# Performance work log

Measured on AMD Instinct MI355X. Metric: run time of the kernel, lower is better.

Reference implementation:

```python
import jax, jax.numpy as jnp
import numpy as np

INF = jnp.float32(1e9)


def _nearest_zero_dist_axis0(is_zero):
    """1D distance (in index units) to the nearest True along axis 0.

    is_zero: bool array [L, ...]. Returns float32 [L, ...].
    """
    d0 = jnp.where(is_zero, jnp.float32(0.0), INF)

    def step(c, d):
        c = jnp.minimum(c + 1.0, d)
        return c, c

    init = jnp.full(d0.shape[1:], INF, dtype=jnp.float32)
    _, fwd = jax.lax.scan(step, init, d0)
    _, bwd = jax.lax.scan(step, init, d0[::-1])
    return jnp.minimum(fwd, bwd[::-1])


def _minplus_parabola_axis0(g2):
    """Exact squared-EDT lower envelope along axis 0.

    g2: float32 [L, ...] of squared distances. Returns
    out[i, ...] = min_k ( (i-k)^2 + g2[k, ...] ).
    Brute-force min-plus, scanned over output index to bound memory.
    """
    L = g2.shape[0]
    k = jnp.arange(L, dtype=jnp.float32)

    def step(_, i):
        # (i - k)^2 broadcast against all source positions k
        par = (i - k) ** 2  # [L]
        par = par.reshape((L,) + (1,) * (g2.ndim - 1))
        return None, jnp.min(par + g2, axis=0)  # [...]

    _, out = jax.lax.scan(step, None, jnp.arange(L, dtype=jnp.float32))
    return out  # [L, ...]


def _edt(x):
    """Exact N-D Euclidean distance transform matching scipy's
    distance_transform_edt: distance from each nonzero element to the
    nearest zero element, over all dims of x."""
    is_zero = (x == 0)
    # Pass 1 (axis 0): exact 1D distance to nearest zero along axis 0.
    d = _nearest_zero_dist_axis0(is_zero)  # [B,H,W]
    d2 = d * d
    # Passes 2..n: exact min-plus with squared parabola along each
    # remaining axis, applied to the running squared distance field.
    for ax in range(1, x.ndim):
        d2 = jnp.moveaxis(d2, ax, 0)
        d2 = _minplus_parabola_axis0(d2)
        d2 = jnp.moveaxis(d2, 0, ax)
    return jnp.sqrt(d2)


def setup_inputs() -> dict:
    key = jax.random.key(0)
    B, H, W = 16, 512, 512
    x = (jax.random.uniform(key, (B, H, W)) > 0.05).astype(jnp.float32)
    return {"x": x}


def reference(x) -> jnp.ndarray:
    distance = _edt(x)
    # distance[x.isnan()] = nan  (NaN inputs are nonzero -> foreground,
    # then their output is masked to NaN, as in the torch module)
    return jnp.where(jnp.isnan(x), jnp.nan, distance)
```

## Files before the change

kernel.cpp:

```cpp
#include <hip/hip_runtime.h>
#include <math.h>
#include <stdint.h>

#define NB 16
#define NH 512
#define NW 512
#define PLANE (NH * NW)
#define INF2 1.0e18f
#define BIG 3.0e38f
#define NSEG 64
#define HROW 516

__device__ __forceinline__ void eval_seg(const float* __restrict__ hrow,
                                         int ss, float* best,
                                         const float* neg2i) {
    const float* hp = hrow + ss * 8;
    float4 A = *reinterpret_cast<const float4*>(hp);
    float4 B = *reinterpret_cast<const float4*>(hp + 4);
    float s8f = (float)(ss * 8);
#pragma unroll
    for (int j = 0; j < 8; ++j) {
        float n2 = neg2i[j];
        float c0 = fmaf(n2, s8f, A.x);
        float c1 = fmaf(n2, s8f + 1.0f, A.y);
        float c2 = fmaf(n2, s8f + 2.0f, A.z);
        float c3 = fmaf(n2, s8f + 3.0f, A.w);
        float c4 = fmaf(n2, s8f + 4.0f, B.x);
        float c5 = fmaf(n2, s8f + 5.0f, B.y);
        float c6 = fmaf(n2, s8f + 6.0f, B.z);
        float c7 = fmaf(n2, s8f + 7.0f, B.w);
        float bb = fminf(fminf(best[j], c0), c1);
        bb = fminf(fminf(bb, c2), c3);
        bb = fminf(fminf(bb, c4), c5);
        bb = fminf(fminf(bb, c6), c7);
        best[j] = bb;
    }
}

__device__ __forceinline__ void eval_window(const float* __restrict__ hrow,
                                            int q, float* best,
                                            const float* neg2i,
                                            const float* ifl) {
    int s_lo0 = (q > 0) ? q - 1 : 0;
    int s_hi0 = (q < NSEG - 1) ? q + 1 : NSEG - 1;
    for (int ss = s_lo0; ss <= s_hi0; ++ss) eval_seg(hrow, ss, best, neg2i);
    float t0 = fmaf(ifl[0], ifl[0], best[0]);
    float t1 = fmaf(ifl[1], ifl[1], best[1]);
    float t2 = fmaf(ifl[2], ifl[2], best[2]);
    float t3 = fmaf(ifl[3], ifl[3], best[3]);
    float t4 = fmaf(ifl[4], ifl[4], best[4]);
    float t5 = fmaf(ifl[5], ifl[5], best[5]);
    float t6 = fmaf(ifl[6], ifl[6], best[6]);
    float t7 = fmaf(ifl[7], ifl[7], best[7]);
    float m = fmaxf(fmaxf(t0, t1), t2);
    m = fmaxf(fmaxf(m, t3), t4);
    m = fmaxf(fmaxf(m, t5), t6);
    float bmax = fmaxf(m, t7);
    int sw = (int)sqrtf(bmax) + 1;
    int i0 = q * 8;
    int s_lo = (i0 - sw) >> 3;
    int s_hi = (i0 + 7 + sw) >> 3;
    if (s_lo < 0) s_lo = 0;
    if (s_hi > NSEG - 1) s_hi = NSEG - 1;
    for (int ss = s_lo; ss <= s_hi; ++ss) {
        if (ss >= s_lo0 && ss <= s_hi0) continue;
        eval_seg(hrow, ss, best, neg2i);
    }
}

__global__ __launch_bounds__(512, 4) void k_scan_h(const float* __restrict__ x,
                                                   unsigned short* __restrict__ code) {
    __shared__ float hs[8 * HROW];
    __shared__ unsigned int flgw[1024];
    __shared__ int lza[512], rza[512];
    int t = threadIdx.x;
    int b = blockIdx.y;
    int w0 = blockIdx.x * 8;
    const float* xb = x + (size_t)b * PLANE + w0;

    for (int m = t; m < 1024; m += 512) {
        int k = m >> 1, half = m & 1;
        float4 v = *reinterpret_cast<const float4*>(xb + (size_t)k * NW + half * 4);
        unsigned int f = 0;
#pragma unroll
        for (int e = 0; e < 4; ++e) {
            float val = (&v.x)[e];
            hs[(half * 4 + e) * HROW + k] = (val == 0.0f) ? 1.0f : 0.0f;
            f |= (isnan(val) ? 1u : 0u) << (8 * e);
        }
        flgw[m] = f;
    }
    __syncthreads();

    int w = t & 7, q = t >> 3;
    int base = w * HROW + q * 8;
    float4 A = *reinterpret_cast<const float4*>(&hs[base]);
    float4 Bv = *reinterpret_cast<const float4*>(&hs[base + 4]);
    unsigned int mask = 0;
#pragma unroll
    for (int e = 0; e < 4; ++e) mask |= ((&A.x)[e] == 1.0f ? 1u : 0u) << e;
#pragma unroll
    for (int e = 0; e < 4; ++e) mask |= ((&Bv.x)[e] == 1.0f ? 1u : 0u) << (e + 4);
    lza[q * 8 + w] = mask ? (q * 8 + __ffs(mask) - 1) : (1 << 20);
    rza[q * 8 + w] = mask ? (q * 8 + 31 - __clz(mask)) : -(1 << 20);

    int fwd[8], bwd[8];
    int run = 1 << 20;
#pragma unroll
    for (int e = 0; e < 8; ++e) { run = ((mask >> e) & 1) ? 0 : run + 1; fwd[e] = run; }
    run = 1 << 20;
#pragma unroll
    for (int e = 7; e >= 0; --e) { run = ((mask >> e) & 1) ? 0 : run + 1; bwd[e] = run; }
    __syncthreads();

    int pmax = -(1 << 20);
    for (int c = 0; c < q; ++c) pmax = max(pmax, rza[c * 8 + w]);
    int smin = 1 << 20;
    for (int c = q + 1; c < 64; ++c) smin = min(smin, lza[c * 8 + w]);

    const unsigned char* flgb = reinterpret_cast<const unsigned char*>(flgw);
#pragma unroll
    for (int e = 0; e < 8; ++e) {
        int i = q * 8 + e;
        int d = min(min(fwd[e], bwd[e]), min(i - pmax, smin - i));
        if (d > 511) d = 1023;
        unsigned short o = (unsigned short)(d | ((flgb[i * 8 + w] & 1) << 15));
        code[(size_t)b * PLANE + (size_t)i * NW + w0 + w] = o;
    }
}

__global__ __launch_bounds__(1024, 2) void k_wb(const unsigned short* __restrict__ code,
                                                float* __restrict__ out) {
    __shared__ float hs[NB * HROW];
    __shared__ unsigned char flg[NB * NW];
    int t = threadIdx.x;
    int h = blockIdx.x;

    const unsigned int* cp = reinterpret_cast<const unsigned int*>(code);
    for (int m = t; m < NB * NW / 2; m += 1024) {
        int b = m >> 8;
        int wp = m & 255;
        unsigned int v = cp[((size_t)b * PLANE + (size_t)h * NW) / 2 + wp];
        int wa = wp * 2;
        int dl0 = v & 1023, dl1 = (v >> 16) & 1023;
        unsigned short fpair = (unsigned short)(((v >> 15) & 1u) | (((v >> 31) & 1u) << 8));
        *reinterpret_cast<unsigned short*>(&flg[b * NW + wa]) = fpair;
        hs[b * HROW + wa] = (dl0 == 1023) ? INF2 : (float)(dl0 * dl0 + wa * wa);
        hs[b * HROW + wa + 1] = (dl1 == 1023) ? INF2 : (float)(dl1 * dl1 + (wa + 1) * (wa + 1));
    }
    __syncthreads();

    int line = t >> 6, q = t & 63;
    int i0 = q * 8;
    float res[8];
    {
        float best[8], neg2i[8], ifl[8];
#pragma unroll
        for (int j = 0; j < 8; ++j) {
            best[j] = BIG;
            ifl[j] = (float)(i0 + j);
            neg2i[j] = (float)(-2 * (i0 + j));
        }
        eval_window(&hs[line * HROW], q, best, neg2i, ifl);
#pragma unroll
        for (int j = 0; j < 8; ++j) res[j] = fmaf(ifl[j], ifl[j], best[j]);
    }
    __syncthreads();
#pragma unroll
    for (int j = 0; j < 8; ++j) hs[line * HROW + i0 + j] = res[j];
    __syncthreads();

    int w = t & 511, g = t >> 9;
    float d2c[NB];
#pragma unroll
    for (int b2 = 0; b2 < NB; ++b2) d2c[b2] = hs[b2 * HROW + w];
#pragma unroll
    for (int j = 0; j < 8; ++j) {
        int bp = g * 8 + j;
        float mm = BIG;
#pragma unroll
        for (int b2 = 0; b2 < NB; ++b2) {
            float db = (float)((bp - b2) * (bp - b2));
            mm = fminf(mm, db + d2c[b2]);
        }
        float sq = sqrtf(mm);
        float o = flg[bp * NW + w] ? __builtin_nanf("") : sq;
        out[(size_t)bp * PLANE + (size_t)h * NW + w] = o;
    }
}

extern "C" void kernel_launch(void* const* d_in, const int* in_sizes, int n_in,
                              void* d_out, int out_size, void* d_ws, size_t ws_size,
                              hipStream_t stream) {
    (void)in_sizes; (void)n_in; (void)out_size; (void)ws_size;
    const float* x = (const float*)d_in[0];
    float* out = (float*)d_out;
    unsigned short* code = (unsigned short*)d_ws;

    k_scan_h<<<dim3(NW / 8, NB), 512, 0, stream>>>(x, code);
    k_wb<<<dim3(NH), 1024, 0, stream>>>(code, out);
}
```

Before: 38.64 us.

## Use wave shuffles for column zero scans and vectorize code stores via LDS transpose

The first kernel now maps one wavefront per column and finds the nearest zeros in earlier and later segments with shuffle-based prefix max/min, replacing serial loops over shared arrays. Per-row results are staged through LDS and written as 16-byte vectors instead of scattered 2-byte stores. The NaN flag is no longer packed into the code; the second kernel re-reads x to apply the NaN mask. This adds a full read of x in the second kernel in exchange for coalesced writes and less LDS work in the first.

```diff
diff --git a/kernel.cpp b/kernel.cpp
--- a/kernel.cpp
+++ b/kernel.cpp
@@ -70,39 +70,31 @@
 
 __global__ __launch_bounds__(512, 4) void k_scan_h(const float* __restrict__ x,
                                                    unsigned short* __restrict__ code) {
-    __shared__ float hs[8 * HROW];
-    __shared__ unsigned int flgw[1024];
-    __shared__ int lza[512], rza[512];
+    __shared__ float ind[8 * HROW];
+    __shared__ unsigned short d16[8 * 520];
     int t = threadIdx.x;
     int b = blockIdx.y;
     int w0 = blockIdx.x * 8;
     const float* xb = x + (size_t)b * PLANE + w0;
 
     for (int m = t; m < 1024; m += 512) {
-        int k = m >> 1, half = m & 1;
-        float4 v = *reinterpret_cast<const float4*>(xb + (size_t)k * NW + half * 4);
-        unsigned int f = 0;
-#pragma unroll
-        for (int e = 0; e < 4; ++e) {
-            float val = (&v.x)[e];
-            hs[(half * 4 + e) * HROW + k] = (val == 0.0f) ? 1.0f : 0.0f;
-            f |= (isnan(val) ? 1u : 0u) << (8 * e);
-        }
-        flgw[m] = f;
-    }
-    __syncthreads();
-
-    int w = t & 7, q = t >> 3;
-    int base = w * HROW + q * 8;
-    float4 A = *reinterpret_cast<const float4*>(&hs[base]);
-    float4 Bv = *reinterpret_cast<const float4*>(&hs[base + 4]);
+        int h = m >> 1, half = m & 1;
+        float4 v = *reinterpret_cast<const float4*>(xb + (size_t)h * NW + half * 4);
+#pragma unroll
+        for (int e = 0; e < 4; ++e)
+            ind[(half * 4 + e) * HROW + h] = ((&v.x)[e] == 0.0f) ? 1.0f : 0.0f;
+    }
+    __syncthreads();
+
+    int w = t >> 6, q = t & 63;
+    const float* col = &ind[w * HROW + q * 8];
+    float4 A = *reinterpret_cast<const float4*>(col);
+    float4 Bv = *reinterpret_cast<const float4*>(col + 4);
     unsigned int mask = 0;
 #pragma unroll
-    for (int e = 0; e < 4; ++e) mask |= ((&A.x)[e] == 1.0f ? 1u : 0u) << e;
-#pragma unroll
-    for (int e = 0; e < 4; ++e) mask |= ((&Bv.x)[e] == 1.0f ? 1u : 0u) << (e + 4);
-    lza[q * 8 + w] = mask ? (q * 8 + __ffs(mask) - 1) : (1 << 20);
-    rza[q * 8 + w] = mask ? (q * 8 + 31 - __clz(mask)) : -(1 << 20);
+    for (int e = 0; e < 4; ++e) mask |= (((&A.x)[e] == 1.0f) ? 1u : 0u) << e;
+#pragma unroll
+    for (int e = 0; e < 4; ++e) mask |= (((&Bv.x)[e] == 1.0f) ? 1u : 0u) << (e + 4);
 
     int fwd[8], bwd[8];
     int run = 1 << 20;
@@ -111,42 +103,71 @@
     run = 1 << 20;
 #pragma unroll
     for (int e = 7; e >= 0; --e) { run = ((mask >> e) & 1) ? 0 : run + 1; bwd[e] = run; }
-    __syncthreads();
-
-    int pmax = -(1 << 20);
-    for (int c = 0; c < q; ++c) pmax = max(pmax, rza[c * 8 + w]);
-    int smin = 1 << 20;
-    for (int c = q + 1; c < 64; ++c) smin = min(smin, lza[c * 8 + w]);
-
-    const unsigned char* flgb = reinterpret_cast<const unsigned char*>(flgw);
+
+    int lz = mask ? (q * 8 + __ffs(mask) - 1) : (1 << 20);
+    int rz = mask ? (q * 8 + 31 - __clz(mask)) : -(1 << 20);
+
+    int pm = rz;
+#pragma unroll
+    for (int d = 1; d < 64; d <<= 1) {
+        int o = __shfl_up(pm, d);
+        if (q >= d) pm = max(pm, o);
+    }
+    int pmax = __shfl_up(pm, 1);
+    if (q == 0) pmax = -(1 << 20);
+    int sm = lz;
+#pragma unroll
+    for (int d = 1; d < 64; d <<= 1) {
+        int o = __shfl_down(sm, d);
+        if (q + d < 64) sm = min(sm, o);
+    }
+    int smin = __shfl_down(sm, 1);
+    if (q == 63) smin = 1 << 20;
+
+    unsigned int dv[8];
 #pragma unroll
     for (int e = 0; e < 8; ++e) {
         int i = q * 8 + e;
-        int d = min(min(fwd[e], bwd[e]), min(i - pmax, smin - i));
-        if (d > 511) d = 1023;
-        unsigned short o = (unsigned short)(d | ((flgb[i * 8 + w] & 1) << 15));
-        code[(size_t)b * PLANE + (size_t)i * NW + w0 + w] = o;
+        int dd = min(min(fwd[e], bwd[e]), min(i - pmax, smin - i));
+        dv[e] = (unsigned int)((dd > 511) ? 1023 : dd);
+    }
+    uint4 pk;
+    pk.x = dv[0] | (dv[1] << 16);
+    pk.y = dv[2] | (dv[3] << 16);
+    pk.z = dv[4] | (dv[5] << 16);
+    pk.w = dv[6] | (dv[7] << 16);
+    *reinterpret_cast<uint4*>(&d16[w * 520 + q * 8]) = pk;
+    __syncthreads();
+
+    {
+        int h = t;
+        unsigned int r[4];
+#pragma unroll
+        for (int p = 0; p < 4; ++p) {
+            unsigned int lo = d16[(2 * p) * 520 + h];
+            unsigned int hi = d16[(2 * p + 1) * 520 + h];
+            r[p] = lo | (hi << 16);
+        }
+        uint4 o; o.x = r[0]; o.y = r[1]; o.z = r[2]; o.w = r[3];
+        *reinterpret_cast<uint4*>(&code[(size_t)b * PLANE + (size_t)h * NW + w0]) = o;
     }
 }
 
 __global__ __launch_bounds__(1024, 2) void k_wb(const unsigned short* __restrict__ code,
+                                                const float* __restrict__ x,
                                                 float* __restrict__ out) {
     __shared__ float hs[NB * HROW];
-    __shared__ unsigned char flg[NB * NW];
     int t = threadIdx.x;
     int h = blockIdx.x;
 
     const unsigned int* cp = reinterpret_cast<const unsigned int*>(code);
     for (int m = t; m < NB * NW / 2; m += 1024) {
-        int b = m >> 8;
-        int wp = m & 255;
+        int b = m >> 8, wp = m & 255;
         unsigned int v = cp[((size_t)b * PLANE + (size_t)h * NW) / 2 + wp];
         int wa = wp * 2;
-        int dl0 = v & 1023, dl1 = (v >> 16) & 1023;
-        unsigned short fpair = (unsigned short)(((v >> 15) & 1u) | (((v >> 31) & 1u) << 8));
-        *reinterpret_cast<unsigned short*>(&flg[b * NW + wa]) = fpair;
-        hs[b * HROW + wa] = (dl0 == 1023) ? INF2 : (float)(dl0 * dl0 + wa * wa);
-        hs[b * HROW + wa + 1] = (dl1 == 1023) ? INF2 : (float)(dl1 * dl1 + (wa + 1) * (wa + 1));
+        int d0 = v & 0xFFFF, d1 = v >> 16;
+        hs[b * HROW + wa] = (d0 == 1023) ? INF2 : (float)(d0 * d0 + wa * wa);
+        hs[b * HROW + wa + 1] = (d1 == 1023) ? INF2 : (float)(d1 * d1 + (wa + 1) * (wa + 1));
     }
     __syncthreads();
 
@@ -173,19 +194,19 @@
     int w = t & 511, g = t >> 9;
     float d2c[NB];
 #pragma unroll
-    for (int b2 = 0; b2 < NB; ++b2) d2c[b2] = hs[b2 * HROW + w];
+    for (int bb = 0; bb < NB; ++bb) d2c[bb] = hs[bb * HROW + w];
 #pragma unroll
     for (int j = 0; j < 8; ++j) {
         int bp = g * 8 + j;
         float mm = BIG;
 #pragma unroll
-        for (int b2 = 0; b2 < NB; ++b2) {
-            float db = (float)((bp - b2) * (bp - b2));
-            mm = fminf(mm, db + d2c[b2]);
+        for (int bb = 0; bb < NB; ++bb) {
+            float db = (float)((bp - bb) * (bp - bb));
+            mm = fminf(mm, db + d2c[bb]);
         }
-        float sq = sqrtf(mm);
-        float o = flg[bp * NW + w] ? __builtin_nanf("") : sq;
-        out[(size_t)bp * PLANE + (size_t)h * NW + w] = o;
+        size_t idx = (size_t)bp * PLANE + (size_t)h * NW + w;
+        float xv = x[idx];
+        out[idx] = isnan(xv) ? __builtin_nanf("") : sqrtf(mm);
     }
 }
 
@@ -198,5 +219,5 @@
     unsigned short* code = (unsigned short*)d_ws;
 
     k_scan_h<<<dim3(NW / 8, NB), 512, 0, stream>>>(x, code);
-    k_wb<<<dim3(NH), 1024, 0, stream>>>(code, out);
-}
+    k_wb<<<dim3(NH), 1024, 0, stream>>>(code, x, out);
+}
```

New measurement: 37.94 us. Within noise of the previous version (-1.8%).
